# Kernel tuning notes

Hardware: AMD Instinct MI355X
Metric: run time of the kernel (lower is better)

Reference implementation:

```python
import jax, jax.numpy as jnp
import numpy as np

DIM = 192
HEADS = 12
HEAD_DIM = DIM // HEADS  # 16
WS = (2, 2, 2)
MLP_HIDDEN = int(2.0 * DIM)
D = H = W = 32
LN_EPS = 1e-5


def setup_inputs() -> dict:
    key = jax.random.key(0)
    ks = jax.random.split(key, 8)
    s = 0.02

    def nrm(k, shape):
        return jax.random.normal(k, shape, jnp.float32) * s

    return {
        "x": jax.random.normal(ks[0], (1, D, H, W, DIM), jnp.float32),
        "xa": jax.random.normal(ks[1], (1, D, H, W, DIM), jnp.float32),
        "norm1_g": jnp.ones((DIM,), jnp.float32),
        "norm1_b": jnp.zeros((DIM,), jnp.float32),
        "norm2_g": jnp.ones((DIM,), jnp.float32),
        "norm2_b": jnp.zeros((DIM,), jnp.float32),
        "Wq": nrm(ks[2], (DIM, DIM)),
        "bq": jnp.zeros((DIM,), jnp.float32),
        "Wkv": nrm(ks[3], (DIM, 2 * DIM)),
        "bkv": jnp.zeros((2 * DIM,), jnp.float32),
        "Wp": nrm(ks[4], (DIM, DIM)),
        "bp": jnp.zeros((DIM,), jnp.float32),
        "W1": nrm(ks[5], (DIM, MLP_HIDDEN)),
        "b1": jnp.zeros((MLP_HIDDEN,), jnp.float32),
        "W2": nrm(ks[6], (MLP_HIDDEN, DIM)),
        "b2": jnp.zeros((DIM,), jnp.float32),
    }


def _ln(x, g, b):
    m = x.mean(-1, keepdims=True)
    v = ((x - m) ** 2).mean(-1, keepdims=True)
    return (x - m) * jax.lax.rsqrt(v + LN_EPS) * g + b


def _window_partition(x):
    # x: (D,H,W,C) -> (nW, N, C), N = prod(WS)
    d, h, w = D // WS[0], H // WS[1], W // WS[2]
    C = x.shape[-1]
    g = x.reshape(d, WS[0], h, WS[1], w, WS[2], C)
    g = g.transpose(0, 2, 4, 1, 3, 5, 6)  # (d,h,w,ws0,ws1,ws2,C)
    return g.reshape(d * h * w, WS[0] * WS[1] * WS[2], C)


def _window_area_partition(x):
    # 3x3x3 neighbor-window expansion with zero padding. Replicates the
    # source bug: neighbor slot 20 (offset (2,0,2)) is left as zeros.
    d, h, w = D // WS[0], H // WS[1], W // WS[2]
    C = x.shape[-1]
    g = x.reshape(d, WS[0], h, WS[1], w, WS[2], C)
    g = g.transpose(0, 2, 4, 1, 3, 5, 6)  # (d,h,w,ws0,ws1,ws2,C)
    p = jnp.pad(g, ((1, 1), (1, 1), (1, 1), (0, 0), (0, 0), (0, 0), (0, 0)))
    slabs = []
    for i in range(27):
        di, dj, dk = i // 9, (i // 3) % 3, i % 3
        if i == 20:
            slabs.append(jnp.zeros_like(g))
        else:
            slabs.append(p[di:di + d, dj:dj + h, dk:dk + w])
    b = jnp.stack(slabs, axis=3)  # (d,h,w,27,ws0,ws1,ws2,C)
    nW = d * h * w
    b = b.reshape(nW, 3, 3, 3, WS[0], WS[1], WS[2], C)
    b = b.transpose(0, 1, 4, 2, 5, 3, 6, 7)  # interleave neighbor/within axes
    return b.reshape(nW, 27 * WS[0] * WS[1] * WS[2], C)


def _window_reverse(win, C):
    # (nW,N,C) -> (D,H,W,C)
    d, h, w = D // WS[0], H // WS[1], W // WS[2]
    x = win.reshape(d, h, w, WS[0], WS[1], WS[2], C)
    x = x.transpose(0, 3, 1, 4, 2, 5, 6)
    return x.reshape(D, H, W, C)


def reference(x, xa, norm1_g, norm1_b, norm2_g, norm2_b,
              Wq, bq, Wkv, bkv, Wp, bp, W1, b1, W2, b2):
    C = DIM
    shortcut = x
    xn = _ln(x[0], norm1_g, norm1_b)
    xan = _ln(xa[0], norm1_g, norm1_b)

    x_win = _window_partition(xn)          # (nW, N, C)
    xa_win = _window_area_partition(xan)   # (nW, 27N, C)
    nW, N, _ = x_win.shape
    M = xa_win.shape[1]

    q = (x_win @ Wq + bq).reshape(nW, N, HEADS, HEAD_DIM)
    kv = (xa_win @ Wkv + bkv).reshape(nW, M, 2, HEADS, HEAD_DIM)
    k, v = kv[:, :, 0], kv[:, :, 1]

    scale = HEAD_DIM ** -0.5
    attn = jnp.einsum('bnhd,bmhd->bhnm', q * scale, k)
    attn = jax.nn.softmax(attn, axis=-1)
    out = jnp.einsum('bhnm,bmhd->bnhd', attn, v).reshape(nW, N, C)
    out = out @ Wp + bp

    x_attn = _window_reverse(out, C)[None]  # (1,D,H,W,C)
    x1 = shortcut + x_attn
    h_mlp = jax.nn.gelu(_ln(x1, norm2_g, norm2_b) @ W1 + b1, approximate=False)
    return x1 + (h_mlp @ W2 + b2)
```

## Files before the change

kernel.cpp:

```cpp
#include <hip/hip_runtime.h>
#include <hip/hip_bf16.h>
#include <math.h>


#define TOK 32768
#define NWIN 4096

typedef float f32x4 __attribute__((ext_vector_type(4)));
typedef short bf16x8 __attribute__((ext_vector_type(8)));
typedef short bf16x4 __attribute__((ext_vector_type(4)));

static __device__ __forceinline__ short f2bf(float x) {
  __hip_bfloat16 h = __float2bfloat16(x);
  return __builtin_bit_cast(short, h);
}

enum { EP_Q = 0, EP_KV = 1, EP_RESID_LN = 2, EP_GELU = 3, EP_RESID = 4 };

static __device__ __forceinline__ void pack_one(const float* __restrict__ W,
                                                short* __restrict__ dst,
                                                int K, int N, int blk, int lane) {
  int KS = K / 32;
  int ks = blk % KS, c = blk / KS;
  int col = c * 16 + (lane & 15);
  int krow = ks * 32 + (lane >> 4) * 8;
  bf16x8 v;
#pragma unroll
  for (int j = 0; j < 8; ++j) v[j] = f2bf(W[(size_t)(krow + j) * N + col]);
  *(bf16x8*)(dst + ((size_t)blk * 64 + lane) * 8) = v;
}

__global__ __launch_bounds__(256) void prep_kernel(
    const float* __restrict__ Wq, const float* __restrict__ Wkv,
    const float* __restrict__ Wp, const float* __restrict__ W1,
    const float* __restrict__ W2, const float* __restrict__ bkv,
    short* __restrict__ wq_p, short* __restrict__ wkv_p, short* __restrict__ wp_p,
    short* __restrict__ w1_p, short* __restrict__ w2_p,
    short* __restrict__ kext, short* __restrict__ vext,
    int* __restrict__ gIdx) {
  int bid = blockIdx.x;
  int tid = threadIdx.x;
  if (bid < 144) {
    int pb = bid * 4 + (tid >> 6);
    int lane = tid & 63;
    if (pb < 72)        pack_one(Wq,  wq_p,  192, 192, pb,       lane);
    else if (pb < 216)  pack_one(Wkv, wkv_p, 192, 384, pb - 72,  lane);
    else if (pb < 288)  pack_one(Wp,  wp_p,  192, 192, pb - 216, lane);
    else if (pb < 432)  pack_one(W1,  w1_p,  192, 384, pb - 288, lane);
    else                pack_one(W2,  w2_p,  384, 192, pb - 432, lane);
  } else if (bid < 144 + NWIN) {
    int w = bid - 144;
    int m = tid;
    if (m >= 224) return;
    int ww = w & 15, wh = (w >> 4) & 15, wd = w >> 8;
    int t = TOK;
    if (m < 216) {
      int lw = m & 1;  int t1 = m >> 1;
      int dk = t1 % 3; int t2 = t1 / 3;
      int lh = t2 & 1; int t3 = t2 >> 1;
      int dj = t3 % 3; int t4 = t3 / 3;
      int ld = t4 & 1; int di = t4 >> 1;
      int nwd = wd + di - 1, nwh = wh + dj - 1, nww = ww + dk - 1;
      int slab = di * 9 + dj * 3 + dk;
      if (nwd >= 0 && nwd <= 15 && nwh >= 0 && nwh <= 15 && nww >= 0 && nww <= 15 && slab != 20) {
        t = ((nwd * 2 + ld) * 32 + (nwh * 2 + lh) ) * 32 + (nww * 2 + lw);
      }
    }
    gIdx[w * 224 + m] = t;
  } else {
    if (tid < 192)      kext[tid] = f2bf(bkv[tid]);
    else if (tid < 384) vext[tid - 192] = f2bf(bkv[tid]);
  }
}

template <int EPI, bool PROLN, int CT, int K, int NTOT>
__global__ __launch_bounds__(256, 2) void gemm_mfma(const void* __restrict__ Av,
                                                    const short* __restrict__ Bp,
                                                    const float* __restrict__ bias,
                                                    const float* __restrict__ resid,
                                                    const float* __restrict__ lg,
                                                    const float* __restrict__ lb,
                                                    void* __restrict__ C0v,
                                                    void* __restrict__ C1v) {
  constexpr int KS = K / 32;
  constexpr int CHUNKS = CT * KS;
  static_assert(CHUNKS == 72);
  __shared__ __align__(16) short Bls[CHUNKS * 512];

  const int lane = threadIdx.x & 63;
  const int wv = threadIdx.x >> 6;
  const int lrow = lane & 15, lkg = lane >> 4;
  const int rb = blockIdx.x * 64 + wv * 16;
  const int nb = blockIdx.y * (CT * 16);
  const int nb16 = blockIdx.y * CT;

  {
    const short* bsrc = Bp + (size_t)nb16 * KS * 512;
#pragma unroll
    for (int i = 0; i < 18; ++i) {
      int ch = wv * 18 + i;
      __builtin_amdgcn_global_load_lds(
          (const __attribute__((address_space(1))) void*)(bsrc + (size_t)ch * 512 + lane * 8),
          (__attribute__((address_space(3))) void*)(Bls + ch * 512), 16, 0, 0);
    }
  }

  bf16x8 af[KS];
  if constexpr (PROLN) {
    const float* Arow = (const float*)Av + (size_t)(rb + lrow) * K + lkg * 8;
    float v[KS][8];
    float s = 0.f;
#pragma unroll
    for (int ks = 0; ks < KS; ++ks) {
      float4 lo = *(const float4*)(Arow + ks * 32);
      float4 hi = *(const float4*)(Arow + ks * 32 + 4);
      v[ks][0] = lo.x; v[ks][1] = lo.y; v[ks][2] = lo.z; v[ks][3] = lo.w;
      v[ks][4] = hi.x; v[ks][5] = hi.y; v[ks][6] = hi.z; v[ks][7] = hi.w;
#pragma unroll
      for (int j = 0; j < 8; ++j) s += v[ks][j];
    }
    s += __shfl_xor(s, 16); s += __shfl_xor(s, 32);
    float mean = s * (1.f / 192.f);
    float vs = 0.f;
#pragma unroll
    for (int ks = 0; ks < KS; ++ks)
#pragma unroll
      for (int j = 0; j < 8; ++j) { float d = v[ks][j] - mean; vs += d * d; }
    vs += __shfl_xor(vs, 16); vs += __shfl_xor(vs, 32);
    float rstd = rsqrtf(vs * (1.f / 192.f) + 1e-5f);
#pragma unroll
    for (int ks = 0; ks < KS; ++ks)
#pragma unroll
      for (int j = 0; j < 8; ++j) {
        int ch = ks * 32 + lkg * 8 + j;
        af[ks][j] = f2bf((v[ks][j] - mean) * rstd * lg[ch] + lb[ch]);
      }
  } else {
    const short* Arow = (const short*)Av + (size_t)(rb + lrow) * K + lkg * 8;
#pragma unroll
    for (int ks = 0; ks < KS; ++ks) af[ks] = *(const bf16x8*)(Arow + ks * 32);
  }

  __syncthreads();

  f32x4 acc[CT];
#pragma unroll
  for (int c = 0; c < CT; ++c) acc[c] = (f32x4){0.f, 0.f, 0.f, 0.f};
#pragma unroll
  for (int ks = 0; ks < KS; ++ks) {
#pragma unroll
    for (int c = 0; c < CT; ++c) {
      bf16x8 bfr = *(const bf16x8*)(Bls + ((c * KS + ks) * 64 + lane) * 8);
      acc[c] = __builtin_amdgcn_mfma_f32_16x16x32_bf16(af[ks], bfr, acc[c], 0, 0, 0);
    }
  }

  if constexpr (EPI == EP_RESID_LN) {
    static_assert(CT == 12);
#pragma unroll
    for (int c = 0; c < 12; ++c) {
      int col = c * 16 + lrow;
      float bia = bias[col];
#pragma unroll
      for (int i = 0; i < 4; ++i) {
        int row = rb + lkg * 4 + i;
        acc[c][i] += bia + resid[(size_t)row * 192 + col];
        ((float*)C0v)[(size_t)row * 192 + col] = acc[c][i];
      }
    }
#pragma unroll
    for (int i = 0; i < 4; ++i) {
      int row = rb + lkg * 4 + i;
      float s2 = 0.f;
#pragma unroll
      for (int c = 0; c < 12; ++c) s2 += acc[c][i];
      s2 += __shfl_xor(s2, 1); s2 += __shfl_xor(s2, 2);
      s2 += __shfl_xor(s2, 4); s2 += __shfl_xor(s2, 8);
      float mean = s2 * (1.f / 192.f);
      float vs2 = 0.f;
#pragma unroll
      for (int c = 0; c < 12; ++c) { float d = acc[c][i] - mean; vs2 += d * d; }
      vs2 += __shfl_xor(vs2, 1); vs2 += __shfl_xor(vs2, 2);
      vs2 += __shfl_xor(vs2, 4); vs2 += __shfl_xor(vs2, 8);
      float rstd = rsqrtf(vs2 * (1.f / 192.f) + 1e-5f);
#pragma unroll
      for (int c = 0; c < 12; ++c) {
        int col = c * 16 + lrow;
        ((short*)C1v)[(size_t)row * 192 + col] =
            f2bf((acc[c][i] - mean) * rstd * lg[col] + lb[col]);
      }
    }
  } else {
#pragma unroll
    for (int c = 0; c < CT; ++c) {
      int col = nb + c * 16 + lrow;
      float bia = bias[col];
#pragma unroll
      for (int i = 0; i < 4; ++i) {
        int row = rb + lkg * 4 + i;
        float v = acc[c][i] + bia;
        if constexpr (EPI == EP_Q) {
          ((short*)C0v)[(size_t)row * NTOT + col] = f2bf(v * 0.36067376022224085f);
        } else if constexpr (EPI == EP_KV) {
          if (col < 192) ((short*)C0v)[(size_t)row * 192 + col] = f2bf(v);
          else           ((short*)C1v)[(size_t)row * 192 + col - 192] = f2bf(v);
        } else if constexpr (EPI == EP_RESID) {
          ((float*)C0v)[(size_t)row * NTOT + col] = v + resid[(size_t)row * NTOT + col];
        } else {
          float gg = 0.5f * v * (1.f + erff(v * 0.70710678118654752f));
          ((short*)C0v)[(size_t)row * NTOT + col] = f2bf(gg);
        }
      }
    }
  }
}

__global__ __launch_bounds__(128, 3) void attn_mfma(const short* __restrict__ qbuf,
                                                    const short* __restrict__ kbuf,
                                                    const short* __restrict__ vbuf,
                                                    const int* __restrict__ gIdx,
                                                    short* __restrict__ obuf) {
  __shared__ __align__(16) short VsS[2][224 * 16];
  __shared__ __align__(16) short PsS[2][8 * 232];

  const int tid = threadIdx.x;
  const int wv = tid >> 6;
  const int lane = tid & 63;
  const int lrow = lane & 15, lkg = lane >> 4;

  unsigned bid = blockIdx.x;
  unsigned u = (bid & 7u) * 3072u + (bid >> 3);
  int w = (int)(u / 6u);
  int h = (int)(u % 6u) * 2 + wv;
  const int ww = w & 15, wh = (w >> 4) & 15, wd = w >> 8;

  short* Vs = VsS[wv];
  short* Ps = PsS[wv];
  const int* gw = gIdx + (size_t)w * 224;

  int ti[14];
#pragma unroll
  for (int T = 0; T < 14; ++T) ti[T] = gw[T * 16 + lrow];
  int mv[14];
#pragma unroll
  for (int k = 0; k < 14; ++k) mv[k] = gw[(lane >> 2) + k * 16];

  bf16x8 qa = (bf16x8)0;
  if (lrow < 8 && lkg < 2) {
    int ldq = lrow >> 2, lhq = (lrow >> 1) & 1, lwq = lrow & 1;
    int tq = ((wd * 2 + ldq) * 32 + (wh * 2 + lhq)) * 32 + (ww * 2 + lwq);
    qa = *(const bf16x8*)(qbuf + (size_t)tq * 192 + h * 16 + lkg * 8);
  }

  bf16x8 kf[14];
#pragma unroll
  for (int T = 0; T < 14; ++T) {
    kf[T] = (bf16x8)0;
    if (lkg < 2)
      kf[T] = *(const bf16x8*)(kbuf + (size_t)ti[T] * 192 + h * 16 + lkg * 8);
  }

  f32x4 s[14];
  const f32x4 zero4 = {0.f, 0.f, 0.f, 0.f};
#pragma unroll
  for (int T = 0; T < 14; ++T)
    s[T] = __builtin_amdgcn_mfma_f32_16x16x32_bf16(qa, kf[T], zero4, 0, 0, 0);
  if (lrow >= 8) {
    s[13][0] = -1e30f; s[13][1] = -1e30f; s[13][2] = -1e30f; s[13][3] = -1e30f;
  }

  const int q4c = (lane & 3) * 4;
  bf16x4 vv[14];
#pragma unroll
  for (int k = 0; k < 14; ++k)
    vv[k] = *(const bf16x4*)(vbuf + (size_t)mv[k] * 192 + h * 16 + q4c);

  float inv[4];
#pragma unroll
  for (int r = 0; r < 4; ++r) {
    float sum = 0.f;
#pragma unroll
    for (int t = 0; t < 14; ++t) {
      float p = exp2f(s[t][r]);
      s[t][r] = p;
      sum += p;
    }
    sum += __shfl_xor(sum, 1);
    sum += __shfl_xor(sum, 2);
    sum += __shfl_xor(sum, 4);
    sum += __shfl_xor(sum, 8);
    inv[r] = 1.f / sum;
  }

  if (lane < 32) {
    const int rbase = (lane >> 4) * 4;
    short* Pw = Ps + lrow;
#pragma unroll
    for (int r = 0; r < 4; ++r)
#pragma unroll
      for (int t = 0; t < 14; ++t)
        Pw[(rbase + r) * 232 + t * 16] = f2bf(s[t][r]);
  }

#pragma unroll
  for (int k = 0; k < 14; ++k)
    *(bf16x4*)(Vs + ((unsigned)lane + (unsigned)k * 64u) * 4u) = vv[k];
  asm volatile("s_waitcnt lgkmcnt(0)" ::: "memory");
  __builtin_amdgcn_sched_barrier(0);

  unsigned vbase = (unsigned)(size_t)((__attribute__((address_space(3))) short*)Vs)
                 + (unsigned)(lkg * 256 + (lrow >> 2) * 32 + (lane & 3) * 8);
  bf16x4 t0[7], t1[7];
#pragma unroll
  for (int T = 0; T < 7; ++T) {
    unsigned a = vbase + (unsigned)(T * 1024);
    asm volatile("ds_read_b64_tr_b16 %0, %1" : "=v"(t0[T]) : "v"(a));
    asm volatile("ds_read_b64_tr_b16 %0, %1 offset:128" : "=v"(t1[T]) : "v"(a));
  }
  bf16x8 pa[7];
#pragma unroll
  for (int T = 0; T < 7; ++T) {
    pa[T] = (bf16x8)0;
    if (lrow < 8) pa[T] = *(const bf16x8*)(Ps + lrow * 232 + T * 32 + lkg * 8);
  }
  asm volatile("s_waitcnt lgkmcnt(0)" ::: "memory");
  __builtin_amdgcn_sched_barrier(0);
  f32x4 o = {0.f, 0.f, 0.f, 0.f};
#pragma unroll
  for (int T = 0; T < 7; ++T) {
    bf16x8 vf = __builtin_shufflevector(t0[T], t1[T], 0, 1, 2, 3, 4, 5, 6, 7);
    o = __builtin_amdgcn_mfma_f32_16x16x32_bf16(pa[T], vf, o, 0, 0, 0);
  }

  if (lane < 32) {
#pragma unroll
    for (int r = 0; r < 4; ++r) {
      int n = (lane >> 4) * 4 + r;
      int ldq = n >> 2, lhq = (n >> 1) & 1, lwq = n & 1;
      int tq = ((wd * 2 + ldq) * 32 + (wh * 2 + lhq)) * 32 + (ww * 2 + lwq);
      obuf[(size_t)tq * 192 + h * 16 + lrow] = f2bf(o[r] * inv[r]);
    }
  }
}

extern "C" void kernel_launch(void* const* d_in, const int* in_sizes, int n_in,
                              void* d_out, int out_size, void* d_ws, size_t ws_size,
                              hipStream_t stream) {
  const float* x   = (const float*)d_in[0];
  const float* xa  = (const float*)d_in[1];
  const float* n1g = (const float*)d_in[2];
  const float* n1b = (const float*)d_in[3];
  const float* n2g = (const float*)d_in[4];
  const float* n2b = (const float*)d_in[5];
  const float* Wq  = (const float*)d_in[6];
  const float* bq  = (const float*)d_in[7];
  const float* Wkv = (const float*)d_in[8];
  const float* bkv = (const float*)d_in[9];
  const float* Wp  = (const float*)d_in[10];
  const float* bp  = (const float*)d_in[11];
  const float* W1  = (const float*)d_in[12];
  const float* b1  = (const float*)d_in[13];
  const float* W2  = (const float*)d_in[14];
  const float* b2  = (const float*)d_in[15];

  char* wsb = (char*)d_ws;
  const size_t BB = (size_t)TOK * 192 * 2;
  short* attn_o = (short*)(wsb + 0 * BB);
  short* xn2    = (short*)(wsb + 1 * BB);
  short* qb     = (short*)(wsb + 2 * BB);
  short* kb     = (short*)(wsb + 3 * BB);
  short* vb     = (short*)(wsb + 4 * BB + 4096);
  float* x1     = (float*)(wsb + 5 * BB + 8192);
  char* p = wsb + 7 * BB + 16384;
  int* gIdx = (int*)p;            p += (size_t)NWIN * 224 * 4;
  short* wq_p  = (short*)p;       p += 192 * 192 * 2;
  short* wkv_p = (short*)p;       p += 192 * 384 * 2;
  short* wp_p  = (short*)p;       p += 192 * 192 * 2;
  short* w1_p  = (short*)p;       p += 192 * 384 * 2;
  short* w2_p  = (short*)p;       p += 384 * 192 * 2;

  short* hmlp = qb;

  prep_kernel<<<144 + NWIN + 1, 256, 0, stream>>>(
      Wq, Wkv, Wp, W1, W2, bkv, wq_p, wkv_p, wp_p, w1_p, w2_p,
      kb + (size_t)TOK * 192, vb + (size_t)TOK * 192, gIdx);

  gemm_mfma<EP_Q, true, 12, 192, 192><<<dim3(512, 1), 256, 0, stream>>>(
      x, wq_p, bq, nullptr, n1g, n1b, qb, nullptr);
  gemm_mfma<EP_KV, true, 12, 192, 384><<<dim3(512, 2), 256, 0, stream>>>(
      xa, wkv_p, bkv, nullptr, n1g, n1b, kb, vb);

  attn_mfma<<<NWIN * 6, 128, 0, stream>>>(qb, kb, vb, gIdx, attn_o);

  gemm_mfma<EP_RESID_LN, false, 12, 192, 192><<<dim3(512, 1), 256, 0, stream>>>(
      attn_o, wp_p, bp, x, n2g, n2b, x1, xn2);

  gemm_mfma<EP_GELU, false, 12, 192, 384><<<dim3(512, 2), 256, 0, stream>>>(
      xn2, w1_p, b1, nullptr, nullptr, nullptr, hmlp, nullptr);
  gemm_mfma<EP_RESID, false, 6, 384, 192><<<dim3(512, 2), 256, 0, stream>>>(
      hmlp, w2_p, b2, x1, nullptr, nullptr, (float*)d_out, nullptr);
}
```

Baseline: 186.1 us.

## Restructure GEMMs to register-held weight fragments and stage attention indices in LDS

Most GEMMs are replaced by a kernel where each wave owns a 48-column slice and holds its weight fragments in registers across four 16-row tiles, dropping the LDS staging of B and the block barrier. The final MLP GEMM now runs over the full K=384 in one block column rather than splitting output columns across blocks. The residual+LayerNorm projection keeps the old LDS design as a dedicated kernel. In attention, gather indices are pre-scaled to byte offsets and loaded once per wave with vector loads into LDS. This trades more register pressure, and for PROLN repeated LN loads per column wave, for fewer LDS round trips.

```diff
diff --git a/kernel.cpp b/kernel.cpp
--- a/kernel.cpp
+++ b/kernel.cpp
@@ -15,7 +15,7 @@
   return __builtin_bit_cast(short, h);
 }
 
-enum { EP_Q = 0, EP_KV = 1, EP_RESID_LN = 2, EP_GELU = 3, EP_RESID = 4 };
+enum { EP_Q = 0, EP_KV = 1, EP_GELU = 3, EP_RESID = 4 };
 
 static __device__ __forceinline__ void pack_one(const float* __restrict__ W,
                                                 short* __restrict__ dst,
@@ -63,142 +63,119 @@
       int nwd = wd + di - 1, nwh = wh + dj - 1, nww = ww + dk - 1;
       int slab = di * 9 + dj * 3 + dk;
       if (nwd >= 0 && nwd <= 15 && nwh >= 0 && nwh <= 15 && nww >= 0 && nww <= 15 && slab != 20) {
-        t = ((nwd * 2 + ld) * 32 + (nwh * 2 + lh) ) * 32 + (nww * 2 + lw);
+        t = ((nwd * 2 + ld) * 32 + (nwh * 2 + lh)) * 32 + (nww * 2 + lw);
       }
     }
-    gIdx[w * 224 + m] = t;
+    gIdx[w * 224 + m] = t * 384;
   } else {
     if (tid < 192)      kext[tid] = f2bf(bkv[tid]);
     else if (tid < 384) vext[tid - 192] = f2bf(bkv[tid]);
   }
 }
 
-template <int EPI, bool PROLN, int CT, int K, int NTOT>
-__global__ __launch_bounds__(256, 2) void gemm_mfma(const void* __restrict__ Av,
-                                                    const short* __restrict__ Bp,
-                                                    const float* __restrict__ bias,
-                                                    const float* __restrict__ resid,
-                                                    const float* __restrict__ lg,
-                                                    const float* __restrict__ lb,
-                                                    void* __restrict__ C0v,
-                                                    void* __restrict__ C1v) {
+template <int EPI, bool PROLN, int KB, int K, int NTOT>
+__global__ __launch_bounds__(256, 2) void gemm_rb(const void* __restrict__ Av,
+                                                  const short* __restrict__ Bp,
+                                                  const float* __restrict__ bias,
+                                                  const float* __restrict__ resid,
+                                                  const float* __restrict__ lg,
+                                                  const float* __restrict__ lb,
+                                                  void* __restrict__ C0v,
+                                                  void* __restrict__ C1v) {
   constexpr int KS = K / 32;
-  constexpr int CHUNKS = CT * KS;
-  static_assert(CHUNKS == 72);
-  __shared__ __align__(16) short Bls[CHUNKS * 512];
-
   const int lane = threadIdx.x & 63;
   const int wv = threadIdx.x >> 6;
   const int lrow = lane & 15, lkg = lane >> 4;
-  const int rb = blockIdx.x * 64 + wv * 16;
-  const int nb = blockIdx.y * (CT * 16);
-  const int nb16 = blockIdx.y * CT;
-
-  {
-    const short* bsrc = Bp + (size_t)nb16 * KS * 512;
-#pragma unroll
-    for (int i = 0; i < 18; ++i) {
-      int ch = wv * 18 + i;
-      __builtin_amdgcn_global_load_lds(
-          (const __attribute__((address_space(1))) void*)(bsrc + (size_t)ch * 512 + lane * 8),
-          (__attribute__((address_space(3))) void*)(Bls + ch * 512), 16, 0, 0);
-    }
-  }
-
-  bf16x8 af[KS];
-  if constexpr (PROLN) {
-    const float* Arow = (const float*)Av + (size_t)(rb + lrow) * K + lkg * 8;
-    float v[KS][8];
-    float s = 0.f;
-#pragma unroll
-    for (int ks = 0; ks < KS; ++ks) {
-      float4 lo = *(const float4*)(Arow + ks * 32);
-      float4 hi = *(const float4*)(Arow + ks * 32 + 4);
-      v[ks][0] = lo.x; v[ks][1] = lo.y; v[ks][2] = lo.z; v[ks][3] = lo.w;
-      v[ks][4] = hi.x; v[ks][5] = hi.y; v[ks][6] = hi.z; v[ks][7] = hi.w;
-#pragma unroll
-      for (int j = 0; j < 8; ++j) s += v[ks][j];
-    }
-    s += __shfl_xor(s, 16); s += __shfl_xor(s, 32);
-    float mean = s * (1.f / 192.f);
-    float vs = 0.f;
-#pragma unroll
-    for (int ks = 0; ks < KS; ++ks)
-#pragma unroll
-      for (int j = 0; j < 8; ++j) { float d = v[ks][j] - mean; vs += d * d; }
-    vs += __shfl_xor(vs, 16); vs += __shfl_xor(vs, 32);
-    float rstd = rsqrtf(vs * (1.f / 192.f) + 1e-5f);
-#pragma unroll
-    for (int ks = 0; ks < KS; ++ks)
-#pragma unroll
-      for (int j = 0; j < 8; ++j) {
-        int ch = ks * 32 + lkg * 8 + j;
-        af[ks][j] = f2bf((v[ks][j] - mean) * rstd * lg[ch] + lb[ch]);
+  const int rb = blockIdx.x * 64;
+  const int cb = blockIdx.y * 192 + wv * 48;
+  const int c16 = cb >> 4;
+
+  f32x4 acc[4][3];
+#pragma unroll
+  for (int mt = 0; mt < 4; ++mt)
+#pragma unroll
+    for (int c3 = 0; c3 < 3; ++c3) acc[mt][c3] = (f32x4){0.f, 0.f, 0.f, 0.f};
+
+#pragma unroll
+  for (int kb = 0; kb < KB; ++kb) {
+    bf16x8 bfr[3][6];
+#pragma unroll
+    for (int c3 = 0; c3 < 3; ++c3)
+#pragma unroll
+      for (int k6 = 0; k6 < 6; ++k6)
+        bfr[c3][k6] = *(const bf16x8*)(Bp + (((size_t)(c16 + c3) * KS + kb * 6 + k6) * 64 + lane) * 8);
+
+    if constexpr (PROLN) {
+#pragma unroll
+      for (int mt = 0; mt < 4; ++mt) {
+        const float* Arow = (const float*)Av + (size_t)(rb + mt * 16 + lrow) * K + lkg * 8;
+        float v[6][8];
+        float s = 0.f;
+#pragma unroll
+        for (int k6 = 0; k6 < 6; ++k6) {
+          float4 lo = *(const float4*)(Arow + k6 * 32);
+          float4 hi = *(const float4*)(Arow + k6 * 32 + 4);
+          v[k6][0] = lo.x; v[k6][1] = lo.y; v[k6][2] = lo.z; v[k6][3] = lo.w;
+          v[k6][4] = hi.x; v[k6][5] = hi.y; v[k6][6] = hi.z; v[k6][7] = hi.w;
+#pragma unroll
+          for (int j = 0; j < 8; ++j) s += v[k6][j];
+        }
+        s += __shfl_xor(s, 16); s += __shfl_xor(s, 32);
+        float mean = s * (1.f / 192.f);
+        float vs = 0.f;
+#pragma unroll
+        for (int k6 = 0; k6 < 6; ++k6)
+#pragma unroll
+          for (int j = 0; j < 8; ++j) { float d = v[k6][j] - mean; vs += d * d; }
+        vs += __shfl_xor(vs, 16); vs += __shfl_xor(vs, 32);
+        float rstd = rsqrtf(vs * (1.f / 192.f) + 1e-5f);
+        bf16x8 af[6];
+#pragma unroll
+        for (int k6 = 0; k6 < 6; ++k6)
+#pragma unroll
+          for (int j = 0; j < 8; ++j) {
+            int ch = k6 * 32 + lkg * 8 + j;
+            af[k6][j] = f2bf((v[k6][j] - mean) * rstd * lg[ch] + lb[ch]);
+          }
+#pragma unroll
+        for (int k6 = 0; k6 < 6; ++k6)
+#pragma unroll
+          for (int c3 = 0; c3 < 3; ++c3)
+            acc[mt][c3] = __builtin_amdgcn_mfma_f32_16x16x32_bf16(af[k6], bfr[c3][k6], acc[mt][c3], 0, 0, 0);
       }
-  } else {
-    const short* Arow = (const short*)Av + (size_t)(rb + lrow) * K + lkg * 8;
-#pragma unroll
-    for (int ks = 0; ks < KS; ++ks) af[ks] = *(const bf16x8*)(Arow + ks * 32);
-  }
-
-  __syncthreads();
-
-  f32x4 acc[CT];
-#pragma unroll
-  for (int c = 0; c < CT; ++c) acc[c] = (f32x4){0.f, 0.f, 0.f, 0.f};
-#pragma unroll
-  for (int ks = 0; ks < KS; ++ks) {
-#pragma unroll
-    for (int c = 0; c < CT; ++c) {
-      bf16x8 bfr = *(const bf16x8*)(Bls + ((c * KS + ks) * 64 + lane) * 8);
-      acc[c] = __builtin_amdgcn_mfma_f32_16x16x32_bf16(af[ks], bfr, acc[c], 0, 0, 0);
-    }
-  }
-
-  if constexpr (EPI == EP_RESID_LN) {
-    static_assert(CT == 12);
-#pragma unroll
-    for (int c = 0; c < 12; ++c) {
-      int col = c * 16 + lrow;
+    } else {
+      bf16x8 af[2][6];
+      {
+        const short* Arow = (const short*)Av + (size_t)(rb + lrow) * K + kb * 192 + lkg * 8;
+#pragma unroll
+        for (int k6 = 0; k6 < 6; ++k6) af[0][k6] = *(const bf16x8*)(Arow + k6 * 32);
+      }
+#pragma unroll
+      for (int mt = 0; mt < 4; ++mt) {
+        if (mt < 3) {
+          const short* Arow = (const short*)Av + (size_t)(rb + (mt + 1) * 16 + lrow) * K + kb * 192 + lkg * 8;
+#pragma unroll
+          for (int k6 = 0; k6 < 6; ++k6) af[(mt + 1) & 1][k6] = *(const bf16x8*)(Arow + k6 * 32);
+        }
+#pragma unroll
+        for (int k6 = 0; k6 < 6; ++k6)
+#pragma unroll
+          for (int c3 = 0; c3 < 3; ++c3)
+            acc[mt][c3] = __builtin_amdgcn_mfma_f32_16x16x32_bf16(af[mt & 1][k6], bfr[c3][k6], acc[mt][c3], 0, 0, 0);
+      }
+    }
+  }
+
+#pragma unroll
+  for (int mt = 0; mt < 4; ++mt)
+#pragma unroll
+    for (int c3 = 0; c3 < 3; ++c3) {
+      int col = cb + c3 * 16 + lrow;
       float bia = bias[col];
 #pragma unroll
       for (int i = 0; i < 4; ++i) {
-        int row = rb + lkg * 4 + i;
-        acc[c][i] += bia + resid[(size_t)row * 192 + col];
-        ((float*)C0v)[(size_t)row * 192 + col] = acc[c][i];
-      }
-    }
-#pragma unroll
-    for (int i = 0; i < 4; ++i) {
-      int row = rb + lkg * 4 + i;
-      float s2 = 0.f;
-#pragma unroll
-      for (int c = 0; c < 12; ++c) s2 += acc[c][i];
-      s2 += __shfl_xor(s2, 1); s2 += __shfl_xor(s2, 2);
-      s2 += __shfl_xor(s2, 4); s2 += __shfl_xor(s2, 8);
-      float mean = s2 * (1.f / 192.f);
-      float vs2 = 0.f;
-#pragma unroll
-      for (int c = 0; c < 12; ++c) { float d = acc[c][i] - mean; vs2 += d * d; }
-      vs2 += __shfl_xor(vs2, 1); vs2 += __shfl_xor(vs2, 2);
-      vs2 += __shfl_xor(vs2, 4); vs2 += __shfl_xor(vs2, 8);
-      float rstd = rsqrtf(vs2 * (1.f / 192.f) + 1e-5f);
-#pragma unroll
-      for (int c = 0; c < 12; ++c) {
-        int col = c * 16 + lrow;
-        ((short*)C1v)[(size_t)row * 192 + col] =
-            f2bf((acc[c][i] - mean) * rstd * lg[col] + lb[col]);
-      }
-    }
-  } else {
-#pragma unroll
-    for (int c = 0; c < CT; ++c) {
-      int col = nb + c * 16 + lrow;
-      float bia = bias[col];
-#pragma unroll
-      for (int i = 0; i < 4; ++i) {
-        int row = rb + lkg * 4 + i;
-        float v = acc[c][i] + bia;
+        int row = rb + mt * 16 + lkg * 4 + i;
+        float v = acc[mt][c3][i] + bia;
         if constexpr (EPI == EP_Q) {
           ((short*)C0v)[(size_t)row * NTOT + col] = f2bf(v * 0.36067376022224085f);
         } else if constexpr (EPI == EP_KV) {
@@ -212,6 +189,81 @@
         }
       }
     }
+}
+
+__global__ __launch_bounds__(256, 2) void gemm_pln2(const short* __restrict__ A,
+                                                    const short* __restrict__ Bp,
+                                                    const float* __restrict__ bias,
+                                                    const float* __restrict__ resid,
+                                                    const float* __restrict__ lg,
+                                                    const float* __restrict__ lb,
+                                                    float* __restrict__ C0,
+                                                    short* __restrict__ C1) {
+  __shared__ __align__(16) short Bls[72 * 512];
+  const int lane = threadIdx.x & 63;
+  const int wv = threadIdx.x >> 6;
+  const int lrow = lane & 15, lkg = lane >> 4;
+  const int rb = blockIdx.x * 64 + wv * 16;
+
+  {
+#pragma unroll
+    for (int i = 0; i < 18; ++i) {
+      int ch = wv * 18 + i;
+      __builtin_amdgcn_global_load_lds(
+          (const __attribute__((address_space(1))) void*)(Bp + (size_t)ch * 512 + lane * 8),
+          (__attribute__((address_space(3))) void*)(Bls + ch * 512), 16, 0, 0);
+    }
+  }
+  bf16x8 af[6];
+  {
+    const short* Arow = A + (size_t)(rb + lrow) * 192 + lkg * 8;
+#pragma unroll
+    for (int ks = 0; ks < 6; ++ks) af[ks] = *(const bf16x8*)(Arow + ks * 32);
+  }
+  __syncthreads();
+
+  f32x4 acc[12];
+#pragma unroll
+  for (int c = 0; c < 12; ++c) acc[c] = (f32x4){0.f, 0.f, 0.f, 0.f};
+#pragma unroll
+  for (int ks = 0; ks < 6; ++ks)
+#pragma unroll
+    for (int c = 0; c < 12; ++c) {
+      bf16x8 bfr = *(const bf16x8*)(Bls + ((c * 6 + ks) * 64 + lane) * 8);
+      acc[c] = __builtin_amdgcn_mfma_f32_16x16x32_bf16(af[ks], bfr, acc[c], 0, 0, 0);
+    }
+
+#pragma unroll
+  for (int c = 0; c < 12; ++c) {
+    int col = c * 16 + lrow;
+    float bia = bias[col];
+#pragma unroll
+    for (int i = 0; i < 4; ++i) {
+      int row = rb + lkg * 4 + i;
+      acc[c][i] += bia + resid[(size_t)row * 192 + col];
+      C0[(size_t)row * 192 + col] = acc[c][i];
+    }
+  }
+#pragma unroll
+  for (int i = 0; i < 4; ++i) {
+    int row = rb + lkg * 4 + i;
+    float s2 = 0.f;
+#pragma unroll
+    for (int c = 0; c < 12; ++c) s2 += acc[c][i];
+    s2 += __shfl_xor(s2, 1); s2 += __shfl_xor(s2, 2);
+    s2 += __shfl_xor(s2, 4); s2 += __shfl_xor(s2, 8);
+    float mean = s2 * (1.f / 192.f);
+    float vs2 = 0.f;
+#pragma unroll
+    for (int c = 0; c < 12; ++c) { float d = acc[c][i] - mean; vs2 += d * d; }
+    vs2 += __shfl_xor(vs2, 1); vs2 += __shfl_xor(vs2, 2);
+    vs2 += __shfl_xor(vs2, 4); vs2 += __shfl_xor(vs2, 8);
+    float rstd = rsqrtf(vs2 * (1.f / 192.f) + 1e-5f);
+#pragma unroll
+    for (int c = 0; c < 12; ++c) {
+      int col = c * 16 + lrow;
+      C1[(size_t)row * 192 + col] = f2bf((acc[c][i] - mean) * rstd * lg[col] + lb[col]);
+    }
   }
 }
 
@@ -236,14 +288,12 @@
 
   short* Vs = VsS[wv];
   short* Ps = PsS[wv];
-  const int* gw = gIdx + (size_t)w * 224;
-
-  int ti[14];
-#pragma unroll
-  for (int T = 0; T < 14; ++T) ti[T] = gw[T * 16 + lrow];
-  int mv[14];
-#pragma unroll
-  for (int k = 0; k < 14; ++k) mv[k] = gw[(lane >> 2) + k * 16];
+
+  int* PsI = (int*)Ps;
+  if (lane < 56) {
+    int4 idx4 = ((const int4*)(gIdx + (size_t)w * 224))[lane];
+    ((int4*)PsI)[lane] = idx4;
+  }
 
   bf16x8 qa = (bf16x8)0;
   if (lrow < 8 && lkg < 2) {
@@ -252,12 +302,19 @@
     qa = *(const bf16x8*)(qbuf + (size_t)tq * 192 + h * 16 + lkg * 8);
   }
 
+  int ti[14];
+#pragma unroll
+  for (int T = 0; T < 14; ++T) ti[T] = PsI[T * 16 + lrow];
+  int mv[14];
+#pragma unroll
+  for (int k = 0; k < 14; ++k) mv[k] = PsI[(lane >> 2) + k * 16];
+
+  const char* kbase = (const char*)kbuf + h * 32 + lkg * 16;
   bf16x8 kf[14];
 #pragma unroll
   for (int T = 0; T < 14; ++T) {
     kf[T] = (bf16x8)0;
-    if (lkg < 2)
-      kf[T] = *(const bf16x8*)(kbuf + (size_t)ti[T] * 192 + h * 16 + lkg * 8);
+    if (lkg < 2) kf[T] = *(const bf16x8*)(kbase + ti[T]);
   }
 
   f32x4 s[14];
@@ -269,11 +326,11 @@
     s[13][0] = -1e30f; s[13][1] = -1e30f; s[13][2] = -1e30f; s[13][3] = -1e30f;
   }
 
-  const int q4c = (lane & 3) * 4;
+  const char* vbase = (const char*)vbuf + h * 32 + (lane & 3) * 8;
   bf16x4 vv[14];
 #pragma unroll
   for (int k = 0; k < 14; ++k)
-    vv[k] = *(const bf16x4*)(vbuf + (size_t)mv[k] * 192 + h * 16 + q4c);
+    vv[k] = *(const bf16x4*)(vbase + mv[k]);
 
   float inv[4];
 #pragma unroll
@@ -308,12 +365,12 @@
   asm volatile("s_waitcnt lgkmcnt(0)" ::: "memory");
   __builtin_amdgcn_sched_barrier(0);
 
-  unsigned vbase = (unsigned)(size_t)((__attribute__((address_space(3))) short*)Vs)
+  unsigned vbadr = (unsigned)(size_t)((__attribute__((address_space(3))) short*)Vs)
                  + (unsigned)(lkg * 256 + (lrow >> 2) * 32 + (lane & 3) * 8);
   bf16x4 t0[7], t1[7];
 #pragma unroll
   for (int T = 0; T < 7; ++T) {
-    unsigned a = vbase + (unsigned)(T * 1024);
+    unsigned a = vbadr + (unsigned)(T * 1024);
     asm volatile("ds_read_b64_tr_b16 %0, %1" : "=v"(t0[T]) : "v"(a));
     asm volatile("ds_read_b64_tr_b16 %0, %1 offset:128" : "=v"(t1[T]) : "v"(a));
   }
@@ -385,18 +442,18 @@
       Wq, Wkv, Wp, W1, W2, bkv, wq_p, wkv_p, wp_p, w1_p, w2_p,
       kb + (size_t)TOK * 192, vb + (size_t)TOK * 192, gIdx);
 
-  gemm_mfma<EP_Q, true, 12, 192, 192><<<dim3(512, 1), 256, 0, stream>>>(
+  gemm_rb<EP_Q, true, 1, 192, 192><<<dim3(512, 1), 256, 0, stream>>>(
       x, wq_p, bq, nullptr, n1g, n1b, qb, nullptr);
-  gemm_mfma<EP_KV, true, 12, 192, 384><<<dim3(512, 2), 256, 0, stream>>>(
+  gemm_rb<EP_KV, true, 1, 192, 384><<<dim3(512, 2), 256, 0, stream>>>(
       xa, wkv_p, bkv, nullptr, n1g, n1b, kb, vb);
 
   attn_mfma<<<NWIN * 6, 128, 0, stream>>>(qb, kb, vb, gIdx, attn_o);
 
-  gemm_mfma<EP_RESID_LN, false, 12, 192, 192><<<dim3(512, 1), 256, 0, stream>>>(
+  gemm_pln2<<<dim3(512, 1), 256, 0, stream>>>(
       attn_o, wp_p, bp, x, n2g, n2b, x1, xn2);
 
-  gemm_mfma<EP_GELU, false, 12, 192, 384><<<dim3(512, 2), 256, 0, stream>>>(
+  gemm_rb<EP_GELU, false, 1, 192, 384><<<dim3(512, 2), 256, 0, stream>>>(
       xn2, w1_p, b1, nullptr, nullptr, nullptr, hmlp, nullptr);
-  gemm_mfma<EP_RESID, false, 6, 384, 192><<<dim3(512, 2), 256, 0, stream>>>(
+  gemm_rb<EP_RESID, false, 2, 384, 192><<<dim3(512, 1), 256, 0, stream>>>(
       hmlp, w2_p, b2, x1, nullptr, nullptr, (float*)d_out, nullptr);
 }
```

Result: slower. 238.6 us (+28.2%).
